# Kernel optimization log

Hardware: AMD Instinct MI355X
Metric: run time of the kernel (lower is better)

Reference implementation:

```python
import jax, jax.numpy as jnp
import numpy as np

B, L, E, H = 8, 1024, 768, 12
D = E // H  # 64 head dim


def _layernorm(x, scale, bias, eps=1e-6):
    m = jnp.mean(x, axis=-1, keepdims=True)
    v = jnp.var(x, axis=-1, keepdims=True)
    return (x - m) * jax.lax.rsqrt(v + eps) * scale + bias


def setup_inputs() -> dict:
    key = jax.random.key(0)
    ks = jax.random.split(key, 8)
    s = lambda fan_in: 1.0 / np.sqrt(fan_in)  # lecun-normal-ish init scale
    return {
        "x": jax.random.normal(ks[0], (B, L, E), jnp.float32),
        "ln1_scale": jnp.ones((E,), jnp.float32),
        "ln1_bias": jnp.zeros((E,), jnp.float32),
        "w_qkv": jax.random.normal(ks[1], (E, 3 * E), jnp.float32) * s(E),
        "b_qkv": jnp.zeros((3 * E,), jnp.float32),
        "w_proj": jax.random.normal(ks[2], (E, E), jnp.float32) * s(E),
        "b_proj": jnp.zeros((E,), jnp.float32),
        "ln2_scale": jnp.ones((E,), jnp.float32),
        "ln2_bias": jnp.zeros((E,), jnp.float32),
        "w_fc": jax.random.normal(ks[3], (E, 4 * E), jnp.float32) * s(E),
        "b_fc": jnp.zeros((4 * E,), jnp.float32),
        "w_out": jax.random.normal(ks[4], (4 * E, E), jnp.float32) * s(4 * E),
        "b_out": jnp.zeros((E,), jnp.float32),
    }


def reference(x, ln1_scale, ln1_bias, w_qkv, b_qkv, w_proj, b_proj,
              ln2_scale, ln2_bias, w_fc, b_fc, w_out, b_out):
    # eval mode: train=False (all dropouts are identity), mask_len=None
    b, l, _ = x.shape
    # ---- pre-LN causal self-attention ----
    z = _layernorm(x, ln1_scale, ln1_bias)
    qkv = z @ w_qkv + b_qkv                                   # (B, L, 3E)
    # faithful to source: reshape to (B, L, H, 3D) then split last axis
    qkv = qkv.reshape(b, l, H, 3 * D).transpose(0, 2, 1, 3)   # (B, H, L, 3D)
    q, k, v = jnp.split(qkv, 3, axis=-1)                      # each (B, H, L, D)
    attn = jnp.einsum("bhqd,bhkd->bhqk", q, k) / jnp.sqrt(jnp.float32(D))
    mask = jnp.tri(l, dtype=jnp.float32)                      # causal lower-tri
    attn = jnp.where(mask == 0, -1e18, attn)
    attn = jax.nn.softmax(attn, axis=-1)
    y = jnp.einsum("bhqk,bhkd->bhqd", attn, v)                # (B, H, L, D)
    y = y.transpose(0, 2, 1, 3).reshape(b, l, E)
    y = y @ w_proj + b_proj
    x = x + y  # residual (resid dropout is identity in eval)
    # ---- MLP block ----
    z = _layernorm(x, ln2_scale, ln2_bias)
    z = jax.nn.selu(z @ w_fc + b_fc) @ w_out + b_out
    return x + z
```

## Files before the change

### kernel.cpp

```cpp
#include <hip/hip_runtime.h>
#include <hip/hip_bf16.h>

typedef __attribute__((ext_vector_type(8))) short short8;
typedef __attribute__((ext_vector_type(4))) float f32x4;
typedef __attribute__((ext_vector_type(4))) unsigned short us4;

#define AS1 __attribute__((address_space(1)))
#define AS3 __attribute__((address_space(3)))

__device__ __forceinline__ unsigned short f2bf(float f) {
    unsigned u = __float_as_uint(f);
    u += 0x7fffu + ((u >> 16) & 1u);
    return (unsigned short)(u >> 16);
}

__device__ __forceinline__ void gload16(const void* g, void* l) {
    __builtin_amdgcn_global_load_lds((AS1 void*)(g), (AS3 void*)(l), 16, 0, 0);
}

__global__ __launch_bounds__(256) void wT_all(const float* __restrict__ w_qkv,
                                              const float* __restrict__ w_proj,
                                              const float* __restrict__ w_fc,
                                              const float* __restrict__ w_out,
                                              unsigned short* __restrict__ wqkvT,
                                              unsigned short* __restrict__ wprojT,
                                              unsigned short* __restrict__ wfcT,
                                              unsigned short* __restrict__ woutT) {
    __shared__ float tile[32][33];
    int id = blockIdx.x;
    const float* in; unsigned short* out; int K, N, bn, bk;
    if (id < 1728)      {            in = w_qkv;  out = wqkvT;  K = 768;  N = 2304; bn = (id % 72) * 32; bk = (id / 72) * 32; }
    else if (id < 2304) { id -= 1728; in = w_proj; out = wprojT; K = 768;  N = 768;  bn = (id % 24) * 32; bk = (id / 24) * 32; }
    else if (id < 4608) { id -= 2304; in = w_fc;   out = wfcT;   K = 768;  N = 3072; bn = (id % 96) * 32; bk = (id / 96) * 32; }
    else                { id -= 4608; in = w_out;  out = woutT;  K = 3072; N = 768;  bn = (id % 24) * 32; bk = (id / 24) * 32; }
    int tx = threadIdx.x & 31, ty = threadIdx.x >> 5;
    #pragma unroll
    for (int i = ty; i < 32; i += 8)
        tile[i][tx] = in[(long)(bk + i) * N + bn + tx];
    __syncthreads();
    #pragma unroll
    for (int i = ty; i < 32; i += 8)
        out[(long)(bn + i) * K + bk + tx] = f2bf(tile[tx][i]);
}

__global__ __launch_bounds__(256) void ln_row(const float* __restrict__ x,
                                              const float* __restrict__ sc,
                                              const float* __restrict__ bi,
                                              unsigned short* __restrict__ z) {
    long row = blockIdx.x;
    const float* xr = x + row * 768;
    int t = threadIdx.x;
    float v0 = xr[t], v1 = xr[t + 256], v2 = xr[t + 512];
    float s = v0 + v1 + v2;
    float ss = v0 * v0 + v1 * v1 + v2 * v2;
    #pragma unroll
    for (int m = 1; m < 64; m <<= 1) { s += __shfl_xor(s, m); ss += __shfl_xor(ss, m); }
    __shared__ float red[8];
    int wid = t >> 6;
    if ((t & 63) == 0) { red[wid] = s; red[4 + wid] = ss; }
    __syncthreads();
    s = red[0] + red[1] + red[2] + red[3];
    ss = red[4] + red[5] + red[6] + red[7];
    float mean = s * (1.f / 768.f);
    float var = fmaxf(ss * (1.f / 768.f) - mean * mean, 0.f);
    float rs = rsqrtf(var + 1e-6f);
    unsigned short* zr = z + row * 768;
    zr[t]       = f2bf((v0 - mean) * rs * sc[t]       + bi[t]);
    zr[t + 256] = f2bf((v1 - mean) * rs * sc[t + 256] + bi[t + 256]);
    zr[t + 512] = f2bf((v2 - mean) * rs * sc[t + 512] + bi[t + 512]);
}

template <int MODE>
__global__ __launch_bounds__(256, 2) void gemm_bf16(
    const unsigned short* __restrict__ A, const unsigned short* __restrict__ Bt,
    const float* __restrict__ bias, const float* __restrict__ resid,
    float* __restrict__ outf, unsigned short* __restrict__ outb,
    unsigned short* __restrict__ vt, int M, int N, int K) {
    __shared__ unsigned short As[128 * 64];
    __shared__ unsigned short Bs[128 * 64];
    const int tid = threadIdx.x, lane = tid & 63, wid = tid >> 6;
    const int wr = wid >> 1, wc = wid & 1;
    const int nwg = gridDim.x * gridDim.y;
    const int orig = blockIdx.y * gridDim.x + blockIdx.x;
    const int swz = (orig & 7) * (nwg >> 3) + (orig >> 3);
    const int bx = swz % gridDim.x, by = swz / gridDim.x;
    const long row0 = (long)by * 128, col0 = (long)bx * 128;

    f32x4 acc[4][4] = {};
    const int nkt = K >> 6;
    for (int t = 0; t < nkt; ++t) {
        #pragma unroll
        for (int kq = 0; kq < 4; kq++) {
            int U = kq * 256 + tid;
            int r = U >> 3, ch = U & 7;
            int kb = (ch * 16) ^ ((r & 7) << 4);
            gload16(A + (row0 + r) * K + t * 64 + (kb >> 1), &As[(kq * 256 + wid * 64) * 8]);
            gload16(Bt + (col0 + r) * K + t * 64 + (kb >> 1), &Bs[(kq * 256 + wid * 64) * 8]);
        }
        __syncthreads();
        #pragma unroll
        for (int kk = 0; kk < 2; kk++) {
            short8 af[4], bf[4];
            #pragma unroll
            for (int m = 0; m < 4; m++) {
                int r = wr * 64 + m * 16 + (lane & 15);
                int off = r * 128 + ((kk * 64 + ((lane >> 4) * 16)) ^ ((r & 7) << 4));
                af[m] = *(const short8*)((const char*)As + off);
            }
            #pragma unroll
            for (int n = 0; n < 4; n++) {
                int r = wc * 64 + n * 16 + (lane & 15);
                int off = r * 128 + ((kk * 64 + ((lane >> 4) * 16)) ^ ((r & 7) << 4));
                bf[n] = *(const short8*)((const char*)Bs + off);
            }
            #pragma unroll
            for (int m = 0; m < 4; m++)
                #pragma unroll
                for (int n = 0; n < 4; n++)
                    acc[m][n] = __builtin_amdgcn_mfma_f32_16x16x32_bf16(af[m], bf[n], acc[m][n], 0, 0, 0);
        }
        __syncthreads();
    }

    const float LAM = 1.0507009873554805f, LAMAL = 1.7580993408473766f;
    #pragma unroll
    for (int n = 0; n < 4; n++) {
        int c = (int)col0 + wc * 64 + n * 16 + (lane & 15);
        float bv = bias[c];
        #pragma unroll
        for (int m = 0; m < 4; m++) {
            long r0 = row0 + wr * 64 + m * 16 + ((lane >> 4) * 4);
            f32x4 v = acc[m][n];
            v += bv;
            if (MODE == 0) {
                int h = c / 192, rem = c - h * 192;
                if (rem < 128) {
                    #pragma unroll
                    for (int r = 0; r < 4; r++) outb[(r0 + r) * 2304 + c] = f2bf(v[r]);
                } else {
                    int d = rem - 128;
                    long bb = r0 >> 10, l = r0 & 1023;
                    us4 p;
                    #pragma unroll
                    for (int r = 0; r < 4; r++) p[r] = f2bf(v[r]);
                    *(us4*)(vt + ((bb * 12 + h) * 64 + d) * 1024 + l) = p;
                }
            } else if (MODE == 1) {
                #pragma unroll
                for (int r = 0; r < 4; r++)
                    outf[(r0 + r) * (long)N + c] = v[r] + resid[(r0 + r) * (long)N + c];
            } else if (MODE == 2) {
                #pragma unroll
                for (int r = 0; r < 4; r++) {
                    float s = v[r];
                    s = s > 0.f ? LAM * s : LAMAL * (__expf(s) - 1.f);
                    outb[(r0 + r) * (long)N + c] = f2bf(s);
                }
            }
        }
    }
}

__global__ __launch_bounds__(256, 2) void attn_kernel(const unsigned short* __restrict__ qkv,
                                                      const unsigned short* __restrict__ vt,
                                                      unsigned short* __restrict__ y) {
    __shared__ unsigned short Qs[128 * 64];
    __shared__ unsigned short Ks[64 * 64];
    __shared__ unsigned short Vs[64 * 64];
    __shared__ unsigned short Ps[4][32 * 64];
    const int tid = threadIdx.x, lane = tid & 63, wid = tid >> 6;
    const int bh = blockIdx.x;
    const int b = bh / 12, h = bh - b * 12;
    const unsigned short* kptr = qkv + (long)b * 1024 * 2304 + h * 192 + 64;
    const unsigned short* vptr = vt + (long)bh * 64 * 1024;

    #pragma unroll
    for (int qi = 0; qi < 2; qi++) {
        const int qt = qi ? (7 - (int)blockIdx.y) : (int)blockIdx.y;
        const long qrow0 = (long)b * 1024 + qt * 128;

        const unsigned short* qptr = qkv + qrow0 * 2304 + h * 192;
        #pragma unroll
        for (int kq = 0; kq < 4; kq++) {
            int U = kq * 256 + tid;
            int r = U >> 3, ch = U & 7;
            int kb = (ch * 16) ^ ((r & 7) << 4);
            gload16(qptr + (long)r * 2304 + (kb >> 1), &Qs[(kq * 256 + wid * 64) * 8]);
        }
        __syncthreads();
        short8 qf[2][2];
        #pragma unroll
        for (int m = 0; m < 2; m++)
            #pragma unroll
            for (int kk = 0; kk < 2; kk++) {
                int r = wid * 32 + m * 16 + (lane & 15);
                int off = r * 128 + ((kk * 64 + ((lane >> 4) * 16)) ^ ((r & 7) << 4));
                qf[m][kk] = *(const short8*)((const char*)Qs + off);
            }

        f32x4 O[2][4] = {};
        float mrow[2][4], lrow[2][4];
        #pragma unroll
        for (int m = 0; m < 2; m++)
            #pragma unroll
            for (int r = 0; r < 4; r++) { mrow[m][r] = -3.0e38f; lrow[m][r] = 0.f; }

        const int qlo = qt * 128 + wid * 32;
        const int nkv = (qt + 1) * 2;

        for (int kvt = 0; kvt < nkv; ++kvt) {
            #pragma unroll
            for (int kq = 0; kq < 2; kq++) {
                int U = kq * 256 + tid;
                int r = U >> 3, ch = U & 7;
                int kb = (ch * 16) ^ ((r & 7) << 4);
                gload16(kptr + (long)(kvt * 64 + r) * 2304 + (kb >> 1), &Ks[(kq * 256 + wid * 64) * 8]);
                gload16(vptr + (long)r * 1024 + kvt * 64 + (kb >> 1), &Vs[(kq * 256 + wid * 64) * 8]);
            }
            __syncthreads();
            if (kvt * 64 <= qlo + 31) {
                f32x4 s[2][4] = {};
                #pragma unroll
                for (int kk = 0; kk < 2; kk++) {
                    short8 kf[4];
                    #pragma unroll
                    for (int n = 0; n < 4; n++) {
                        int r = n * 16 + (lane & 15);
                        int off = r * 128 + ((kk * 64 + ((lane >> 4) * 16)) ^ ((r & 7) << 4));
                        kf[n] = *(const short8*)((const char*)Ks + off);
                    }
                    #pragma unroll
                    for (int m = 0; m < 2; m++)
                        #pragma unroll
                        for (int n = 0; n < 4; n++)
                            s[m][n] = __builtin_amdgcn_mfma_f32_16x16x32_bf16(qf[m][kk], kf[n], s[m][n], 0, 0, 0);
                }
                const bool needmask = (kvt * 64 + 63) > qlo;
                #pragma unroll
                for (int m = 0; m < 2; m++)
                    #pragma unroll
                    for (int n = 0; n < 4; n++) {
                        s[m][n] = s[m][n] * 0.125f;
                        if (needmask) {
                            int c = kvt * 64 + n * 16 + (lane & 15);
                            #pragma unroll
                            for (int r = 0; r < 4; r++) {
                                int rr = qlo + m * 16 + ((lane >> 4) * 4) + r;
                                if (c > rr) s[m][n][r] = -1.0e30f;
                            }
                        }
                    }
                #pragma unroll
                for (int m = 0; m < 2; m++)
                    #pragma unroll
                    for (int r = 0; r < 4; r++) {
                        float mx = fmaxf(fmaxf(s[m][0][r], s[m][1][r]), fmaxf(s[m][2][r], s[m][3][r]));
                        #pragma unroll
                        for (int msk = 1; msk < 16; msk <<= 1) mx = fmaxf(mx, __shfl_xor(mx, msk));
                        float mnew = fmaxf(mrow[m][r], mx);
                        float al = __expf(mrow[m][r] - mnew);
                        float ps = 0.f;
                        #pragma unroll
                        for (int n = 0; n < 4; n++) {
                            float p = __expf(s[m][n][r] - mnew);
                            s[m][n][r] = p;
                            ps += p;
                        }
                        #pragma unroll
                        for (int msk = 1; msk < 16; msk <<= 1) ps += __shfl_xor(ps, msk);
                        lrow[m][r] = lrow[m][r] * al + ps;
                        mrow[m][r] = mnew;
                        #pragma unroll
                        for (int n = 0; n < 4; n++) O[m][n][r] *= al;
                    }
                unsigned short* pw = Ps[wid];
                #pragma unroll
                for (int m = 0; m < 2; m++)
                    #pragma unroll
                    for (int n = 0; n < 4; n++)
                        #pragma unroll
                        for (int r = 0; r < 4; r++) {
                            int pr = m * 16 + ((lane >> 4) * 4) + r;
                            int off = (pr * 128 + (n * 16 + (lane & 15)) * 2) ^ ((pr & 7) << 4);
                            *(unsigned short*)((char*)pw + off) = f2bf(s[m][n][r]);
                        }
                #pragma unroll
                for (int kk = 0; kk < 2; kk++) {
                    short8 pf[2], vf[4];
                    #pragma unroll
                    for (int m = 0; m < 2; m++) {
                        int r = m * 16 + (lane & 15);
                        int off = r * 128 + ((kk * 64 + ((lane >> 4) * 16)) ^ ((r & 7) << 4));
                        pf[m] = *(const short8*)((const char*)pw + off);
                    }
                    #pragma unroll
                    for (int n = 0; n < 4; n++) {
                        int r = n * 16 + (lane & 15);
                        int off = r * 128 + ((kk * 64 + ((lane >> 4) * 16)) ^ ((r & 7) << 4));
                        vf[n] = *(const short8*)((const char*)Vs + off);
                    }
                    #pragma unroll
                    for (int m = 0; m < 2; m++)
                        #pragma unroll
                        for (int n = 0; n < 4; n++)
                            O[m][n] = __builtin_amdgcn_mfma_f32_16x16x32_bf16(pf[m], vf[n], O[m][n], 0, 0, 0);
                }
            }
            __syncthreads();
        }
        unsigned short* yb = y + (qrow0 + wid * 32) * 768 + h * 64;
        #pragma unroll
        for (int m = 0; m < 2; m++)
            #pragma unroll
            for (int n = 0; n < 4; n++)
                #pragma unroll
                for (int r = 0; r < 4; r++) {
                    int rr = m * 16 + ((lane >> 4) * 4) + r;
                    yb[(long)rr * 768 + n * 16 + (lane & 15)] = f2bf(O[m][n][r] / lrow[m][r]);
                }
    }
}

extern "C" void kernel_launch(void* const* d_in, const int* in_sizes, int n_in,
                              void* d_out, int out_size, void* d_ws, size_t ws_size,
                              hipStream_t stream) {
    (void)in_sizes; (void)n_in; (void)out_size; (void)ws_size;
    const float* x      = (const float*)d_in[0];
    const float* ln1_s  = (const float*)d_in[1];
    const float* ln1_b  = (const float*)d_in[2];
    const float* w_qkv  = (const float*)d_in[3];
    const float* b_qkv  = (const float*)d_in[4];
    const float* w_proj = (const float*)d_in[5];
    const float* b_proj = (const float*)d_in[6];
    const float* ln2_s  = (const float*)d_in[7];
    const float* ln2_b  = (const float*)d_in[8];
    const float* w_fc   = (const float*)d_in[9];
    const float* b_fc   = (const float*)d_in[10];
    const float* w_out  = (const float*)d_in[11];
    const float* b_out  = (const float*)d_in[12];

    unsigned short* wqkvT = (unsigned short*)d_ws;
    unsigned short* wprojT = wqkvT + (size_t)2304 * 768;
    unsigned short* wfcT   = wprojT + (size_t)768 * 768;
    unsigned short* woutT  = wfcT + (size_t)3072 * 768;
    unsigned short* zbuf   = woutT + (size_t)768 * 3072;
    unsigned short* qkvb   = zbuf + (size_t)8192 * 768;
    unsigned short* vtb    = qkvb + (size_t)8192 * 2304;
    unsigned short* abuf   = qkvb;
    float* x2 = (float*)(vtb + (size_t)96 * 64 * 1024);

    wT_all<<<6912, 256, 0, stream>>>(w_qkv, w_proj, w_fc, w_out, wqkvT, wprojT, wfcT, woutT);

    ln_row<<<8192, 256, 0, stream>>>(x, ln1_s, ln1_b, zbuf);
    gemm_bf16<0><<<dim3(18, 64), 256, 0, stream>>>(zbuf, wqkvT, b_qkv, nullptr, nullptr, qkvb, vtb, 8192, 2304, 768);
    attn_kernel<<<dim3(96, 4), 256, 0, stream>>>(qkvb, vtb, zbuf);
    gemm_bf16<1><<<dim3(6, 64), 256, 0, stream>>>(zbuf, wprojT, b_proj, x, x2, nullptr, nullptr, 8192, 768, 768);
    ln_row<<<8192, 256, 0, stream>>>(x2, ln2_s, ln2_b, zbuf);
    gemm_bf16<2><<<dim3(24, 64), 256, 0, stream>>>(zbuf, wfcT, b_fc, nullptr, nullptr, abuf, nullptr, 8192, 3072, 768);
    gemm_bf16<1><<<dim3(6, 64), 256, 0, stream>>>(abuf, woutT, b_out, x2, (float*)d_out, nullptr, nullptr, 8192, 768, 3072);
}
```

Measured before the change: 386.8 us.

## Double-buffer K/V in attention, split query tiles per block, fuse prelude kernels

The attention kernel now processes one query tile per block, scheduled heaviest-first over a 96x8 grid, and double-buffers K/V tiles in LDS so the next tile's global loads overlap the current tile's compute. Q is staged in the P scratch buffer to keep the LDS footprint within budget. The weight transpose and the first layernorm are merged into a single launch to remove one kernel launch. In exchange, it drops the paired causal load balancing and relies on hand-placed vmcnt waits and barriers being correct.

```diff
diff --git a/kernel.cpp b/kernel.cpp
--- a/kernel.cpp
+++ b/kernel.cpp
@@ -18,29 +18,57 @@
     __builtin_amdgcn_global_load_lds((AS1 void*)(g), (AS3 void*)(l), 16, 0, 0);
 }
 
-__global__ __launch_bounds__(256) void wT_all(const float* __restrict__ w_qkv,
-                                              const float* __restrict__ w_proj,
-                                              const float* __restrict__ w_fc,
-                                              const float* __restrict__ w_out,
-                                              unsigned short* __restrict__ wqkvT,
-                                              unsigned short* __restrict__ wprojT,
-                                              unsigned short* __restrict__ wfcT,
-                                              unsigned short* __restrict__ woutT) {
+__global__ __launch_bounds__(256) void prelude(const float* __restrict__ w_qkv,
+                                               const float* __restrict__ w_proj,
+                                               const float* __restrict__ w_fc,
+                                               const float* __restrict__ w_out,
+                                               unsigned short* __restrict__ wqkvT,
+                                               unsigned short* __restrict__ wprojT,
+                                               unsigned short* __restrict__ wfcT,
+                                               unsigned short* __restrict__ woutT,
+                                               const float* __restrict__ x,
+                                               const float* __restrict__ sc,
+                                               const float* __restrict__ bi,
+                                               unsigned short* __restrict__ z) {
     __shared__ float tile[32][33];
     int id = blockIdx.x;
-    const float* in; unsigned short* out; int K, N, bn, bk;
-    if (id < 1728)      {            in = w_qkv;  out = wqkvT;  K = 768;  N = 2304; bn = (id % 72) * 32; bk = (id / 72) * 32; }
-    else if (id < 2304) { id -= 1728; in = w_proj; out = wprojT; K = 768;  N = 768;  bn = (id % 24) * 32; bk = (id / 24) * 32; }
-    else if (id < 4608) { id -= 2304; in = w_fc;   out = wfcT;   K = 768;  N = 3072; bn = (id % 96) * 32; bk = (id / 96) * 32; }
-    else                { id -= 4608; in = w_out;  out = woutT;  K = 3072; N = 768;  bn = (id % 24) * 32; bk = (id / 24) * 32; }
-    int tx = threadIdx.x & 31, ty = threadIdx.x >> 5;
-    #pragma unroll
-    for (int i = ty; i < 32; i += 8)
-        tile[i][tx] = in[(long)(bk + i) * N + bn + tx];
-    __syncthreads();
-    #pragma unroll
-    for (int i = ty; i < 32; i += 8)
-        out[(long)(bn + i) * K + bk + tx] = f2bf(tile[tx][i]);
+    if (id < 6912) {
+        const float* in; unsigned short* out; int K, N, bn, bk;
+        if (id < 1728)      {            in = w_qkv;  out = wqkvT;  K = 768;  N = 2304; bn = (id % 72) * 32; bk = (id / 72) * 32; }
+        else if (id < 2304) { id -= 1728; in = w_proj; out = wprojT; K = 768;  N = 768;  bn = (id % 24) * 32; bk = (id / 24) * 32; }
+        else if (id < 4608) { id -= 2304; in = w_fc;   out = wfcT;   K = 768;  N = 3072; bn = (id % 96) * 32; bk = (id / 96) * 32; }
+        else                { id -= 4608; in = w_out;  out = woutT;  K = 3072; N = 768;  bn = (id % 24) * 32; bk = (id / 24) * 32; }
+        int tx = threadIdx.x & 31, ty = threadIdx.x >> 5;
+        #pragma unroll
+        for (int i = ty; i < 32; i += 8)
+            tile[i][tx] = in[(long)(bk + i) * N + bn + tx];
+        __syncthreads();
+        #pragma unroll
+        for (int i = ty; i < 32; i += 8)
+            out[(long)(bn + i) * K + bk + tx] = f2bf(tile[tx][i]);
+    } else {
+        long row = id - 6912;
+        const float* xr = x + row * 768;
+        int t = threadIdx.x;
+        float v0 = xr[t], v1 = xr[t + 256], v2 = xr[t + 512];
+        float s = v0 + v1 + v2;
+        float ss = v0 * v0 + v1 * v1 + v2 * v2;
+        #pragma unroll
+        for (int m = 1; m < 64; m <<= 1) { s += __shfl_xor(s, m); ss += __shfl_xor(ss, m); }
+        int wid = t >> 6;
+        float* red = &tile[0][0];
+        if ((t & 63) == 0) { red[wid] = s; red[4 + wid] = ss; }
+        __syncthreads();
+        s = red[0] + red[1] + red[2] + red[3];
+        ss = red[4] + red[5] + red[6] + red[7];
+        float mean = s * (1.f / 768.f);
+        float var = fmaxf(ss * (1.f / 768.f) - mean * mean, 0.f);
+        float rs = rsqrtf(var + 1e-6f);
+        unsigned short* zr = z + row * 768;
+        zr[t]       = f2bf((v0 - mean) * rs * sc[t]       + bi[t]);
+        zr[t + 256] = f2bf((v1 - mean) * rs * sc[t + 256] + bi[t + 256]);
+        zr[t + 512] = f2bf((v2 - mean) * rs * sc[t + 512] + bi[t + 512]);
+    }
 }
 
 __global__ __launch_bounds__(256) void ln_row(const float* __restrict__ x,
@@ -164,161 +192,169 @@
 __global__ __launch_bounds__(256, 2) void attn_kernel(const unsigned short* __restrict__ qkv,
                                                       const unsigned short* __restrict__ vt,
                                                       unsigned short* __restrict__ y) {
-    __shared__ unsigned short Qs[128 * 64];
-    __shared__ unsigned short Ks[64 * 64];
-    __shared__ unsigned short Vs[64 * 64];
+    __shared__ unsigned short Kd[2][64 * 64];
+    __shared__ unsigned short Vd[2][64 * 64];
     __shared__ unsigned short Ps[4][32 * 64];
     const int tid = threadIdx.x, lane = tid & 63, wid = tid >> 6;
     const int bh = blockIdx.x;
+    const int qt = 7 - (int)blockIdx.y;
     const int b = bh / 12, h = bh - b * 12;
     const unsigned short* kptr = qkv + (long)b * 1024 * 2304 + h * 192 + 64;
     const unsigned short* vptr = vt + (long)bh * 64 * 1024;
-
-    #pragma unroll
-    for (int qi = 0; qi < 2; qi++) {
-        const int qt = qi ? (7 - (int)blockIdx.y) : (int)blockIdx.y;
-        const long qrow0 = (long)b * 1024 + qt * 128;
-
-        const unsigned short* qptr = qkv + qrow0 * 2304 + h * 192;
-        #pragma unroll
-        for (int kq = 0; kq < 4; kq++) {
+    const long qrow0 = (long)b * 1024 + qt * 128;
+
+    auto stageKV = [&](int buf, int kvt) {
+        #pragma unroll
+        for (int kq = 0; kq < 2; kq++) {
             int U = kq * 256 + tid;
             int r = U >> 3, ch = U & 7;
             int kb = (ch * 16) ^ ((r & 7) << 4);
-            gload16(qptr + (long)r * 2304 + (kb >> 1), &Qs[(kq * 256 + wid * 64) * 8]);
-        }
-        __syncthreads();
-        short8 qf[2][2];
-        #pragma unroll
-        for (int m = 0; m < 2; m++)
+            gload16(kptr + (long)(kvt * 64 + r) * 2304 + (kb >> 1), &Kd[buf][(kq * 256 + wid * 64) * 8]);
+            gload16(vptr + (long)r * 1024 + kvt * 64 + (kb >> 1), &Vd[buf][(kq * 256 + wid * 64) * 8]);
+        }
+    };
+
+    unsigned short* Qs = &Ps[0][0];
+    const unsigned short* qptr = qkv + qrow0 * 2304 + h * 192;
+    #pragma unroll
+    for (int kq = 0; kq < 4; kq++) {
+        int U = kq * 256 + tid;
+        int r = U >> 3, ch = U & 7;
+        int kb = (ch * 16) ^ ((r & 7) << 4);
+        gload16(qptr + (long)r * 2304 + (kb >> 1), &Qs[(kq * 256 + wid * 64) * 8]);
+    }
+    stageKV(0, 0);
+    asm volatile("s_waitcnt vmcnt(0)" ::: "memory");
+    __builtin_amdgcn_s_barrier();
+    short8 qf[2][2];
+    #pragma unroll
+    for (int m = 0; m < 2; m++)
+        #pragma unroll
+        for (int kk = 0; kk < 2; kk++) {
+            int r = wid * 32 + m * 16 + (lane & 15);
+            int off = r * 128 + ((kk * 64 + ((lane >> 4) * 16)) ^ ((r & 7) << 4));
+            qf[m][kk] = *(const short8*)((const char*)Qs + off);
+        }
+
+    f32x4 O[2][4] = {};
+    float mrow[2][4], lrow[2][4];
+    #pragma unroll
+    for (int m = 0; m < 2; m++)
+        #pragma unroll
+        for (int r = 0; r < 4; r++) { mrow[m][r] = -3.0e38f; lrow[m][r] = 0.f; }
+
+    const int qlo = qt * 128 + wid * 32;
+    const int nkv = (qt + 1) * 2;
+
+    for (int kvt = 0; kvt < nkv; ++kvt) {
+        const int cur = kvt & 1;
+        const bool pf = (kvt + 1 < nkv);
+        if (pf) stageKV(cur ^ 1, kvt + 1);
+        if (pf) asm volatile("s_waitcnt vmcnt(4)" ::: "memory");
+        else    asm volatile("s_waitcnt vmcnt(0)" ::: "memory");
+        __builtin_amdgcn_s_barrier();
+        if (kvt * 64 <= qlo + 31) {
+            const unsigned short* Ks = &Kd[cur][0];
+            const unsigned short* Vs = &Vd[cur][0];
+            f32x4 s[2][4] = {};
             #pragma unroll
             for (int kk = 0; kk < 2; kk++) {
-                int r = wid * 32 + m * 16 + (lane & 15);
-                int off = r * 128 + ((kk * 64 + ((lane >> 4) * 16)) ^ ((r & 7) << 4));
-                qf[m][kk] = *(const short8*)((const char*)Qs + off);
-            }
-
-        f32x4 O[2][4] = {};
-        float mrow[2][4], lrow[2][4];
-        #pragma unroll
-        for (int m = 0; m < 2; m++)
-            #pragma unroll
-            for (int r = 0; r < 4; r++) { mrow[m][r] = -3.0e38f; lrow[m][r] = 0.f; }
-
-        const int qlo = qt * 128 + wid * 32;
-        const int nkv = (qt + 1) * 2;
-
-        for (int kvt = 0; kvt < nkv; ++kvt) {
-            #pragma unroll
-            for (int kq = 0; kq < 2; kq++) {
-                int U = kq * 256 + tid;
-                int r = U >> 3, ch = U & 7;
-                int kb = (ch * 16) ^ ((r & 7) << 4);
-                gload16(kptr + (long)(kvt * 64 + r) * 2304 + (kb >> 1), &Ks[(kq * 256 + wid * 64) * 8]);
-                gload16(vptr + (long)r * 1024 + kvt * 64 + (kb >> 1), &Vs[(kq * 256 + wid * 64) * 8]);
-            }
-            __syncthreads();
-            if (kvt * 64 <= qlo + 31) {
-                f32x4 s[2][4] = {};
-                #pragma unroll
-                for (int kk = 0; kk < 2; kk++) {
-                    short8 kf[4];
-                    #pragma unroll
-                    for (int n = 0; n < 4; n++) {
-                        int r = n * 16 + (lane & 15);
-                        int off = r * 128 + ((kk * 64 + ((lane >> 4) * 16)) ^ ((r & 7) << 4));
-                        kf[n] = *(const short8*)((const char*)Ks + off);
-                    }
-                    #pragma unroll
-                    for (int m = 0; m < 2; m++)
+                short8 kf[4];
+                #pragma unroll
+                for (int n = 0; n < 4; n++) {
+                    int r = n * 16 + (lane & 15);
+                    int off = r * 128 + ((kk * 64 + ((lane >> 4) * 16)) ^ ((r & 7) << 4));
+                    kf[n] = *(const short8*)((const char*)Ks + off);
+                }
+                #pragma unroll
+                for (int m = 0; m < 2; m++)
+                    #pragma unroll
+                    for (int n = 0; n < 4; n++)
+                        s[m][n] = __builtin_amdgcn_mfma_f32_16x16x32_bf16(qf[m][kk], kf[n], s[m][n], 0, 0, 0);
+            }
+            const bool needmask = (kvt * 64 + 63) > qlo;
+            #pragma unroll
+            for (int m = 0; m < 2; m++)
+                #pragma unroll
+                for (int n = 0; n < 4; n++) {
+                    s[m][n] = s[m][n] * 0.125f;
+                    if (needmask) {
+                        int c = kvt * 64 + n * 16 + (lane & 15);
                         #pragma unroll
-                        for (int n = 0; n < 4; n++)
-                            s[m][n] = __builtin_amdgcn_mfma_f32_16x16x32_bf16(qf[m][kk], kf[n], s[m][n], 0, 0, 0);
-                }
-                const bool needmask = (kvt * 64 + 63) > qlo;
-                #pragma unroll
-                for (int m = 0; m < 2; m++)
-                    #pragma unroll
-                    for (int n = 0; n < 4; n++) {
-                        s[m][n] = s[m][n] * 0.125f;
-                        if (needmask) {
-                            int c = kvt * 64 + n * 16 + (lane & 15);
-                            #pragma unroll
-                            for (int r = 0; r < 4; r++) {
-                                int rr = qlo + m * 16 + ((lane >> 4) * 4) + r;
-                                if (c > rr) s[m][n][r] = -1.0e30f;
-                            }
+                        for (int r = 0; r < 4; r++) {
+                            int rr = qlo + m * 16 + ((lane >> 4) * 4) + r;
+                            if (c > rr) s[m][n][r] = -1.0e30f;
                         }
                     }
+                }
+            #pragma unroll
+            for (int m = 0; m < 2; m++)
+                #pragma unroll
+                for (int r = 0; r < 4; r++) {
+                    float mx = fmaxf(fmaxf(s[m][0][r], s[m][1][r]), fmaxf(s[m][2][r], s[m][3][r]));
+                    #pragma unroll
+                    for (int msk = 1; msk < 16; msk <<= 1) mx = fmaxf(mx, __shfl_xor(mx, msk));
+                    float mnew = fmaxf(mrow[m][r], mx);
+                    float al = __expf(mrow[m][r] - mnew);
+                    float ps = 0.f;
+                    #pragma unroll
+                    for (int n = 0; n < 4; n++) {
+                        float p = __expf(s[m][n][r] - mnew);
+                        s[m][n][r] = p;
+                        ps += p;
+                    }
+                    #pragma unroll
+                    for (int msk = 1; msk < 16; msk <<= 1) ps += __shfl_xor(ps, msk);
+                    lrow[m][r] = lrow[m][r] * al + ps;
+                    mrow[m][r] = mnew;
+                    #pragma unroll
+                    for (int n = 0; n < 4; n++) O[m][n][r] *= al;
+                }
+            unsigned short* pw = Ps[wid];
+            #pragma unroll
+            for (int m = 0; m < 2; m++)
+                #pragma unroll
+                for (int n = 0; n < 4; n++)
+                    #pragma unroll
+                    for (int r = 0; r < 4; r++) {
+                        int pr = m * 16 + ((lane >> 4) * 4) + r;
+                        int off = (pr * 128 + (n * 16 + (lane & 15)) * 2) ^ ((pr & 7) << 4);
+                        *(unsigned short*)((char*)pw + off) = f2bf(s[m][n][r]);
+                    }
+            #pragma unroll
+            for (int kk = 0; kk < 2; kk++) {
+                short8 pf2[2], vf[4];
+                #pragma unroll
+                for (int m = 0; m < 2; m++) {
+                    int r = m * 16 + (lane & 15);
+                    int off = r * 128 + ((kk * 64 + ((lane >> 4) * 16)) ^ ((r & 7) << 4));
+                    pf2[m] = *(const short8*)((const char*)pw + off);
+                }
+                #pragma unroll
+                for (int n = 0; n < 4; n++) {
+                    int r = n * 16 + (lane & 15);
+                    int off = r * 128 + ((kk * 64 + ((lane >> 4) * 16)) ^ ((r & 7) << 4));
+                    vf[n] = *(const short8*)((const char*)Vs + off);
+                }
                 #pragma unroll
                 for (int m = 0; m < 2; m++)
                     #pragma unroll
-                    for (int r = 0; r < 4; r++) {
-                        float mx = fmaxf(fmaxf(s[m][0][r], s[m][1][r]), fmaxf(s[m][2][r], s[m][3][r]));
-                        #pragma unroll
-                        for (int msk = 1; msk < 16; msk <<= 1) mx = fmaxf(mx, __shfl_xor(mx, msk));
-                        float mnew = fmaxf(mrow[m][r], mx);
-                        float al = __expf(mrow[m][r] - mnew);
-                        float ps = 0.f;
-                        #pragma unroll
-                        for (int n = 0; n < 4; n++) {
-                            float p = __expf(s[m][n][r] - mnew);
-                            s[m][n][r] = p;
-                            ps += p;
-                        }
-                        #pragma unroll
-                        for (int msk = 1; msk < 16; msk <<= 1) ps += __shfl_xor(ps, msk);
-                        lrow[m][r] = lrow[m][r] * al + ps;
-                        mrow[m][r] = mnew;
-                        #pragma unroll
-                        for (int n = 0; n < 4; n++) O[m][n][r] *= al;
-                    }
-                unsigned short* pw = Ps[wid];
-                #pragma unroll
-                for (int m = 0; m < 2; m++)
-                    #pragma unroll
                     for (int n = 0; n < 4; n++)
-                        #pragma unroll
-                        for (int r = 0; r < 4; r++) {
-                            int pr = m * 16 + ((lane >> 4) * 4) + r;
-                            int off = (pr * 128 + (n * 16 + (lane & 15)) * 2) ^ ((pr & 7) << 4);
-                            *(unsigned short*)((char*)pw + off) = f2bf(s[m][n][r]);
-                        }
-                #pragma unroll
-                for (int kk = 0; kk < 2; kk++) {
-                    short8 pf[2], vf[4];
-                    #pragma unroll
-                    for (int m = 0; m < 2; m++) {
-                        int r = m * 16 + (lane & 15);
-                        int off = r * 128 + ((kk * 64 + ((lane >> 4) * 16)) ^ ((r & 7) << 4));
-                        pf[m] = *(const short8*)((const char*)pw + off);
-                    }
-                    #pragma unroll
-                    for (int n = 0; n < 4; n++) {
-                        int r = n * 16 + (lane & 15);
-                        int off = r * 128 + ((kk * 64 + ((lane >> 4) * 16)) ^ ((r & 7) << 4));
-                        vf[n] = *(const short8*)((const char*)Vs + off);
-                    }
-                    #pragma unroll
-                    for (int m = 0; m < 2; m++)
-                        #pragma unroll
-                        for (int n = 0; n < 4; n++)
-                            O[m][n] = __builtin_amdgcn_mfma_f32_16x16x32_bf16(pf[m], vf[n], O[m][n], 0, 0, 0);
-                }
-            }
-            __syncthreads();
-        }
-        unsigned short* yb = y + (qrow0 + wid * 32) * 768 + h * 64;
-        #pragma unroll
-        for (int m = 0; m < 2; m++)
-            #pragma unroll
-            for (int n = 0; n < 4; n++)
-                #pragma unroll
-                for (int r = 0; r < 4; r++) {
-                    int rr = m * 16 + ((lane >> 4) * 4) + r;
-                    yb[(long)rr * 768 + n * 16 + (lane & 15)] = f2bf(O[m][n][r] / lrow[m][r]);
-                }
-    }
+                        O[m][n] = __builtin_amdgcn_mfma_f32_16x16x32_bf16(pf2[m], vf[n], O[m][n], 0, 0, 0);
+            }
+        }
+        __builtin_amdgcn_s_barrier();
+    }
+    unsigned short* yb = y + (qrow0 + wid * 32) * 768 + h * 64;
+    #pragma unroll
+    for (int m = 0; m < 2; m++)
+        #pragma unroll
+        for (int n = 0; n < 4; n++)
+            #pragma unroll
+            for (int r = 0; r < 4; r++) {
+                int rr = m * 16 + ((lane >> 4) * 4) + r;
+                yb[(long)rr * 768 + n * 16 + (lane & 15)] = f2bf(O[m][n][r] / lrow[m][r]);
+            }
 }
 
 extern "C" void kernel_launch(void* const* d_in, const int* in_sizes, int n_in,
@@ -349,11 +385,10 @@
     unsigned short* abuf   = qkvb;
     float* x2 = (float*)(vtb + (size_t)96 * 64 * 1024);
 
-    wT_all<<<6912, 256, 0, stream>>>(w_qkv, w_proj, w_fc, w_out, wqkvT, wprojT, wfcT, woutT);
-
-    ln_row<<<8192, 256, 0, stream>>>(x, ln1_s, ln1_b, zbuf);
+    prelude<<<15104, 256, 0, stream>>>(w_qkv, w_proj, w_fc, w_out, wqkvT, wprojT, wfcT, woutT,
+                                       x, ln1_s, ln1_b, zbuf);
     gemm_bf16<0><<<dim3(18, 64), 256, 0, stream>>>(zbuf, wqkvT, b_qkv, nullptr, nullptr, qkvb, vtb, 8192, 2304, 768);
-    attn_kernel<<<dim3(96, 4), 256, 0, stream>>>(qkvb, vtb, zbuf);
+    attn_kernel<<<dim3(96, 8), 256, 0, stream>>>(qkvb, vtb, zbuf);
     gemm_bf16<1><<<dim3(6, 64), 256, 0, stream>>>(zbuf, wprojT, b_proj, x, x2, nullptr, nullptr, 8192, 768, 768);
     ln_row<<<8192, 256, 0, stream>>>(x2, ln2_s, ln2_b, zbuf);
     gemm_bf16<2><<<dim3(24, 64), 256, 0, stream>>>(zbuf, wfcT, b_fc, nullptr, nullptr, abuf, nullptr, 8192, 3072, 768);
```

After: 364.3 us. 5.8% less time.
